# Optimization experiments

Measured on AMD Instinct MI355X. Metric: run time of the kernel, lower is better.

Reference implementation:

```python
import jax, jax.numpy as jnp
import numpy as np

THETA = 5.0  # cache sharpness (init arg `theta`)
D_FEAT = 2048
N_MEM = 200000
N_CLASSES = 1000


def setup_inputs() -> dict:
    key = jax.random.key(0)
    k1, k2, k3 = jax.random.split(key, 3)
    x = jax.random.normal(k1, (1, D_FEAT), dtype=jnp.float32)  # backbone output
    mem_keys = jax.random.normal(k2, (D_FEAT, N_MEM), dtype=jnp.float32)
    mem_vals = jax.random.uniform(k3, (N_MEM, N_CLASSES), dtype=jnp.float32)
    return {"x": x, "mem_keys": mem_keys, "mem_vals": mem_vals}


def reference(x, mem_keys, mem_vals):
    # squeeze -> [D]; global L2 normalize (torch.norm over whole tensor)
    v = jnp.squeeze(x)
    v = v / jnp.linalg.norm(v)
    # single-query unnormalized attention over the memory bank
    similarities = jnp.exp(THETA * (v @ mem_keys))   # [N_MEM]
    p_mem = similarities @ mem_vals                  # [N_CLASSES]
    return jnp.log(p_mem).reshape(1, N_CLASSES)
```

## Files before the change

### kernel.cpp

```cpp
#include <hip/hip_runtime.h>
#include <math.h>

#define D_FEAT    2048
#define N_MEM     200000
#define N_CLASSES 1000
#define NC4       (N_CLASSES / 4)
#define THETA     5.0f
#define BLK       256

__global__ __launch_bounds__(BLK) void cache_fused_kernel(
    const float* __restrict__ x,
    const float* __restrict__ K,
    const float* __restrict__ V,
    float*       __restrict__ acc)
{
    __shared__ float x_lds[D_FEAT];
    __shared__ float sims[BLK];
    __shared__ float wred[BLK / 64];

    const int t = threadIdx.x;

    float ss = 0.f;
    #pragma unroll
    for (int k = 0; k < D_FEAT / BLK; ++k) {
        float v = x[t + k * BLK];
        x_lds[t + k * BLK] = v;
        ss += v * v;
    }
    #pragma unroll
    for (int off = 32; off >= 1; off >>= 1)
        ss += __shfl_xor(ss, off, 64);
    if ((t & 63) == 0) wred[t >> 6] = ss;
    __syncthreads();
    const float scale = THETA / sqrtf(wred[0] + wred[1] + wred[2] + wred[3]);

    const int j0 = blockIdx.x * BLK;
    const int j  = j0 + t;
    float dot = 0.f;
    if (j < N_MEM) {
        const float* kp = K + j;
        float a0 = 0.f, a1 = 0.f, a2 = 0.f, a3 = 0.f;
        for (int d = 0; d < D_FEAT; d += 4) {
            a0 = fmaf(x_lds[d + 0], kp[(size_t)(d + 0) * N_MEM], a0);
            a1 = fmaf(x_lds[d + 1], kp[(size_t)(d + 1) * N_MEM], a1);
            a2 = fmaf(x_lds[d + 2], kp[(size_t)(d + 2) * N_MEM], a2);
            a3 = fmaf(x_lds[d + 3], kp[(size_t)(d + 3) * N_MEM], a3);
        }
        dot = (a0 + a1) + (a2 + a3);
        sims[t] = expf(scale * dot);
    }
    __syncthreads();

    const int jcnt = min(BLK, N_MEM - j0);
    if (t < NC4) {
        float4 a = make_float4(0.f, 0.f, 0.f, 0.f);
        const float4* Vp = (const float4*)V + (size_t)j0 * NC4 + t;
        for (int jj = 0; jj < jcnt; ++jj) {
            const float  s  = sims[jj];
            const float4 vv = Vp[(size_t)jj * NC4];
            a.x = fmaf(s, vv.x, a.x);
            a.y = fmaf(s, vv.y, a.y);
            a.z = fmaf(s, vv.z, a.z);
            a.w = fmaf(s, vv.w, a.w);
        }
        atomicAdd(&acc[t * 4 + 0], a.x);
        atomicAdd(&acc[t * 4 + 1], a.y);
        atomicAdd(&acc[t * 4 + 2], a.z);
        atomicAdd(&acc[t * 4 + 3], a.w);
    }
}

__global__ void log_inplace_kernel(float* __restrict__ out)
{
    const int c = blockIdx.x * blockDim.x + threadIdx.x;
    if (c < N_CLASSES) out[c] = logf(out[c]);
}

extern "C" void kernel_launch(void* const* d_in, const int* in_sizes, int n_in,
                              void* d_out, int out_size, void* d_ws, size_t ws_size,
                              hipStream_t stream)
{
    const float* x = (const float*)d_in[0];
    const float* K = (const float*)d_in[1];
    const float* V = (const float*)d_in[2];
    float* out = (float*)d_out;

    hipMemsetAsync(out, 0, N_CLASSES * sizeof(float), stream);

    const int grid = (N_MEM + BLK - 1) / BLK;
    cache_fused_kernel<<<grid, BLK, 0, stream>>>(x, K, V, out);
    log_inplace_kernel<<<(N_CLASSES + 255) / 256, 256, 0, stream>>>(out);
}
```

Before: 489.8 us.

## Split K dot-product across warps by D chunks with float4 column loads

Each block now has its four wavefronts each handle a quarter of the feature dimension. Every thread loads four adjacent memory columns as a float4, and the partial sums are reduced through shared memory before the exp. This shortens each thread's serial dependency chain and widens the global loads on the 1.6 GB key matrix, aiming for more memory-level parallelism. The costs are an extra LDS reduction step and a barrier, and only 64 threads compute the exp stage.

Result: faster. 480.0 us (-2.0%).

```diff
diff --git a/kernel.cpp b/kernel.cpp
--- a/kernel.cpp
+++ b/kernel.cpp
@@ -7,6 +7,9 @@
 #define NC4       (N_CLASSES / 4)
 #define THETA     5.0f
 #define BLK       256
+#define COLS      256
+#define DCHUNK    (D_FEAT / 4)
+#define NM4       (N_MEM / 4)
 
 __global__ __launch_bounds__(BLK) void cache_fused_kernel(
     const float* __restrict__ x,
@@ -14,18 +17,20 @@
     const float* __restrict__ V,
     float*       __restrict__ acc)
 {
-    __shared__ float x_lds[D_FEAT];
-    __shared__ float sims[BLK];
-    __shared__ float wred[BLK / 64];
+    __shared__ float  x_lds[D_FEAT];
+    __shared__ float4 partl[4][64];
+    __shared__ float  sims[COLS];
+    __shared__ float  wred[BLK / 64];
 
     const int t = threadIdx.x;
 
     float ss = 0.f;
+    const float4* x4 = (const float4*)x;
     #pragma unroll
-    for (int k = 0; k < D_FEAT / BLK; ++k) {
-        float v = x[t + k * BLK];
-        x_lds[t + k * BLK] = v;
-        ss += v * v;
+    for (int k = 0; k < D_FEAT / 4 / BLK; ++k) {
+        float4 v = x4[t + k * BLK];
+        ((float4*)x_lds)[t + k * BLK] = v;
+        ss += v.x * v.x + v.y * v.y + v.z * v.z + v.w * v.w;
     }
     #pragma unroll
     for (int off = 32; off >= 1; off >>= 1)
@@ -34,39 +39,53 @@
     __syncthreads();
     const float scale = THETA / sqrtf(wred[0] + wred[1] + wred[2] + wred[3]);
 
-    const int j0 = blockIdx.x * BLK;
-    const int j  = j0 + t;
-    float dot = 0.f;
-    if (j < N_MEM) {
-        const float* kp = K + j;
-        float a0 = 0.f, a1 = 0.f, a2 = 0.f, a3 = 0.f;
-        for (int d = 0; d < D_FEAT; d += 4) {
-            a0 = fmaf(x_lds[d + 0], kp[(size_t)(d + 0) * N_MEM], a0);
-            a1 = fmaf(x_lds[d + 1], kp[(size_t)(d + 1) * N_MEM], a1);
-            a2 = fmaf(x_lds[d + 2], kp[(size_t)(d + 2) * N_MEM], a2);
-            a3 = fmaf(x_lds[d + 3], kp[(size_t)(d + 3) * N_MEM], a3);
+    const int tx = t & 63;
+    const int ty = t >> 6;
+    const int j0 = (int)blockIdx.x * COLS;
+    const int jq = j0 + tx * 4;
+    float4 a = make_float4(0.f, 0.f, 0.f, 0.f);
+    if (jq < N_MEM) {
+        const float4* kp = (const float4*)(K + (size_t)ty * DCHUNK * N_MEM + jq);
+        const float*  xp = x_lds + ty * DCHUNK;
+        #pragma unroll 8
+        for (int dd = 0; dd < DCHUNK; ++dd) {
+            const float  xv = xp[dd];
+            const float4 kv = kp[(size_t)dd * NM4];
+            a.x = fmaf(xv, kv.x, a.x);
+            a.y = fmaf(xv, kv.y, a.y);
+            a.z = fmaf(xv, kv.z, a.z);
+            a.w = fmaf(xv, kv.w, a.w);
         }
-        dot = (a0 + a1) + (a2 + a3);
-        sims[t] = expf(scale * dot);
+    }
+    partl[ty][tx] = a;
+    __syncthreads();
+
+    if (t < 64) {
+        const float4 s0 = partl[0][t], s1 = partl[1][t];
+        const float4 s2 = partl[2][t], s3 = partl[3][t];
+        sims[t * 4 + 0] = expf(scale * ((s0.x + s1.x) + (s2.x + s3.x)));
+        sims[t * 4 + 1] = expf(scale * ((s0.y + s1.y) + (s2.y + s3.y)));
+        sims[t * 4 + 2] = expf(scale * ((s0.z + s1.z) + (s2.z + s3.z)));
+        sims[t * 4 + 3] = expf(scale * ((s0.w + s1.w) + (s2.w + s3.w)));
     }
     __syncthreads();
 
-    const int jcnt = min(BLK, N_MEM - j0);
+    const int jcnt = min(COLS, N_MEM - j0);
     if (t < NC4) {
-        float4 a = make_float4(0.f, 0.f, 0.f, 0.f);
+        float4 a4 = make_float4(0.f, 0.f, 0.f, 0.f);
         const float4* Vp = (const float4*)V + (size_t)j0 * NC4 + t;
         for (int jj = 0; jj < jcnt; ++jj) {
             const float  s  = sims[jj];
             const float4 vv = Vp[(size_t)jj * NC4];
-            a.x = fmaf(s, vv.x, a.x);
-            a.y = fmaf(s, vv.y, a.y);
-            a.z = fmaf(s, vv.z, a.z);
-            a.w = fmaf(s, vv.w, a.w);
+            a4.x = fmaf(s, vv.x, a4.x);
+            a4.y = fmaf(s, vv.y, a4.y);
+            a4.z = fmaf(s, vv.z, a4.z);
+            a4.w = fmaf(s, vv.w, a4.w);
         }
-        atomicAdd(&acc[t * 4 + 0], a.x);
-        atomicAdd(&acc[t * 4 + 1], a.y);
-        atomicAdd(&acc[t * 4 + 2], a.z);
-        atomicAdd(&acc[t * 4 + 3], a.w);
+        atomicAdd(&acc[t * 4 + 0], a4.x);
+        atomicAdd(&acc[t * 4 + 1], a4.y);
+        atomicAdd(&acc[t * 4 + 2], a4.z);
+        atomicAdd(&acc[t * 4 + 3], a4.w);
     }
 }
 
@@ -87,7 +106,7 @@
 
     hipMemsetAsync(out, 0, N_CLASSES * sizeof(float), stream);
 
-    const int grid = (N_MEM + BLK - 1) / BLK;
+    const int grid = (N_MEM + COLS - 1) / COLS;
     cache_fused_kernel<<<grid, BLK, 0, stream>>>(x, K, V, out);
     log_inplace_kernel<<<(N_CLASSES + 255) / 256, 256, 0, stream>>>(out);
 }
```
